# Kernel optimization log

Hardware: AMD Instinct MI355X
Metric: run time of the kernel (lower is better)

The kernel has to match this reference:

```python
import jax, jax.numpy as jnp
import numpy as np

N_HEAD = 16
NEG_BIG = 1e10  # matches the module's -10000000000.0 masking constant


def setup_inputs() -> dict:
    key = jax.random.key(0)
    k1, k2, k3 = jax.random.split(key, 3)
    B, S, D = 2, 2048, 1024
    std = 0.02
    return {
        "x": jax.random.normal(k1, (B, S, D), dtype=jnp.float32),
        "c_attn_w": jax.random.normal(k2, (D, 3 * D), dtype=jnp.float32) * std,
        "c_attn_b": jnp.zeros((3 * D,), dtype=jnp.float32),
        "c_proj_w": jax.random.normal(k3, (D, D), dtype=jnp.float32) * std,
        "c_proj_b": jnp.zeros((D,), dtype=jnp.float32),
    }


def reference(x, c_attn_w, c_attn_b, c_proj_w, c_proj_b):
    B, S, D = x.shape
    H = N_HEAD
    Dh = D // H

    # c_attn: fused QKV projection (Conv1D == linear)
    qkv = jnp.einsum("bsd,df->bsf", x, c_attn_w) + c_attn_b  # [B,S,3D]
    q, k, v = jnp.split(qkv, 3, axis=-1)

    def split_heads(t):  # [B,S,D] -> [B,H,S,Dh]
        return t.reshape(B, S, H, Dh).transpose(0, 2, 1, 3)

    q, k, v = split_heads(q), split_heads(k), split_heads(v)
    present = jnp.stack([k, v], axis=1)  # [B,2,H,S,Dh]

    # scores: explicit O(S^2) matrix, scaled by sqrt(head_dim)
    w = jnp.einsum("bhqd,bhkd->bhqk", q, k) / jnp.sqrt(
        jnp.asarray(Dh, dtype=q.dtype)
    )  # [B,H,S,S]

    # causal mask, applied exactly as in the source: w*mask - 1e10*(1-mask)
    mask = jnp.tril(jnp.ones((S, S), dtype=w.dtype))[None, None]  # [1,1,S,S]
    w = w * mask - NEG_BIG * (1.0 - mask)

    w = jax.nn.softmax(w, axis=-1)
    a = jnp.einsum("bhqk,bhkd->bhqd", w, v)  # [B,H,S,Dh]

    # merge heads: [B,H,S,Dh] -> [B,S,D]
    a = a.transpose(0, 2, 1, 3).reshape(B, S, D)

    # output projection
    a = jnp.einsum("bsd,df->bsf", a, c_proj_w) + c_proj_b
    return (a, present)
```

## Files before the change

kernel.cpp:

```cpp
#include <hip/hip_runtime.h>
#include <hip/hip_bf16.h>
#include <stdint.h>

typedef __bf16 bf16_t;
typedef __bf16 bf16x8 __attribute__((ext_vector_type(8)));
typedef __bf16 bf16x4v __attribute__((ext_vector_type(4)));
typedef float f32x4 __attribute__((ext_vector_type(4)));

#define MFMA16(A, B, C) __builtin_amdgcn_mfma_f32_16x16x32_bf16((A), (B), (C), 0, 0, 0)

#define BB 2
#define SS 2048
#define DD 1024
#define HH 16
#define DH 64
#define MM (BB * SS)

__device__ __forceinline__ void load_lds16(const void* g, void* l) {
  __builtin_amdgcn_global_load_lds(
      (const __attribute__((address_space(1))) void*)g,
      (__attribute__((address_space(3))) void*)l, 16, 0, 0);
}

__device__ __forceinline__ float fast_exp2(float x) {
  float r;
  asm("v_exp_f32 %0, %1" : "=v"(r) : "v"(x));
  return r;
}
__device__ __forceinline__ uint32_t cvt_pk_bf16(float lo, float hi) {
  uint32_t u;
  asm("v_cvt_pk_bf16_f32 %0, %1, %2" : "=v"(u) : "v"(lo), "v"(hi));
  return u;
}


__global__ __launch_bounds__(256) void cvt_f32_to_bf16(const float* __restrict__ in,
                                                       bf16_t* __restrict__ out, int n4) {
  int i = blockIdx.x * blockDim.x + threadIdx.x;
  if (i >= n4) return;
  float4 v = reinterpret_cast<const float4*>(in)[i];
  bf16x4v o;
  o[0] = (bf16_t)v.x; o[1] = (bf16_t)v.y; o[2] = (bf16_t)v.z; o[3] = (bf16_t)v.w;
  reinterpret_cast<bf16x4v*>(out)[i] = o;
}

__global__ void transpose_f32_to_bf16(const float* __restrict__ W, bf16_t* __restrict__ WT,
                                      int K, int N) {
  __shared__ float tile[32][33];
  int n0 = blockIdx.x * 32, k0 = blockIdx.y * 32;
  int tx = threadIdx.x, ty = threadIdx.y;
  #pragma unroll
  for (int i = ty; i < 32; i += 8) tile[i][tx] = W[(size_t)(k0 + i) * N + n0 + tx];
  __syncthreads();
  #pragma unroll
  for (int i = ty; i < 32; i += 8) WT[(size_t)(n0 + i) * K + k0 + tx] = (bf16_t)tile[tx][i];
}

template <int EPI>
__global__ __launch_bounds__(256) void gemm_bf16(
    const bf16_t* __restrict__ A, const bf16_t* __restrict__ BT,
    const float* __restrict__ bias, float* __restrict__ outf,
    bf16_t* __restrict__ q_b, bf16_t* __restrict__ k_b, bf16_t* __restrict__ vt_b,
    int M, int N, int K) {
  __shared__ __align__(16) bf16_t At[2][128 * 32];
  __shared__ __align__(16) bf16_t Bt[2][128 * 32];

  const int tid = threadIdx.x;
  const int l = tid & 63, w = tid >> 6;
  const int lr = l & 15, lg = l >> 4;
  const int wr = w >> 1, wc = w & 1;
  const int row0 = blockIdx.y * 128, col0 = blockIdx.x * 128;

  auto stage = [&](int buf, int k0) {
    #pragma unroll
    for (int i = 0; i < 2; ++i) {
      int e = (tid + i * 256) * 8;
      int r = e >> 5, c = e & 31;
      int base = (w * 64 + i * 256) * 8;
      load_lds16(&A[(size_t)(row0 + r) * K + k0 + c], &At[buf][base]);
      load_lds16(&BT[(size_t)(col0 + r) * K + k0 + c], &Bt[buf][base]);
    }
  };

  f32x4 vz = {0.f, 0.f, 0.f, 0.f};
  f32x4 acc[4][4];
  #pragma unroll
  for (int m = 0; m < 4; ++m)
    #pragma unroll
    for (int n = 0; n < 4; ++n) acc[m][n] = vz;

  stage(0, 0);
  __syncthreads();
  int cur = 0;
  for (int k0 = 0; k0 < K; k0 += 32) {
    if (k0 + 32 < K) stage(cur ^ 1, k0 + 32);
    bf16x8 af[4], bfr[4];
    #pragma unroll
    for (int m = 0; m < 4; ++m)
      af[m] = *(const bf16x8*)&At[cur][(wr * 64 + m * 16 + lr) * 32 + lg * 8];
    #pragma unroll
    for (int n = 0; n < 4; ++n)
      bfr[n] = *(const bf16x8*)&Bt[cur][(wc * 64 + n * 16 + lr) * 32 + lg * 8];
    #pragma unroll
    for (int m = 0; m < 4; ++m)
      #pragma unroll
      for (int n = 0; n < 4; ++n) acc[m][n] = MFMA16(af[m], bfr[n], acc[m][n]);
    __syncthreads();
    cur ^= 1;
  }

  #pragma unroll
  for (int m = 0; m < 4; ++m) {
    int rl = wr * 64 + m * 16 + lg * 4;
    #pragma unroll
    for (int n = 0; n < 4; ++n) {
      int col = col0 + wc * 64 + n * 16 + lr;
      float bz = bias[col];
      #pragma unroll
      for (int r = 0; r < 4; ++r) {
        int row = row0 + rl + r;
        float v = acc[m][n][r] + bz;
        if (EPI == 1) {
          outf[(size_t)row * N + col] = v;
        } else {
          int b = row >> 11, s = row & 2047;
          int part = col >> 10, d = col & 1023;
          int h = d >> 6, dh = d & 63;
          size_t idx = ((size_t)(b * HH + h) * SS + s) * DH + dh;
          if (part == 0) {
            q_b[idx] = (bf16_t)v;
          } else if (part == 1) {
            k_b[idx] = (bf16_t)v;
            outf[(((size_t)(b * 2 + 0) * HH + h) * SS + s) * DH + dh] = v;
          } else {
            vt_b[((size_t)(b * HH + h) * DH + dh) * SS + s] = (bf16_t)v;
            outf[(((size_t)(b * 2 + 1) * HH + h) * SS + s) * DH + dh] = v;
          }
        }
      }
    }
  }
}

__global__ __launch_bounds__(256) void attn_fwd(
    const bf16_t* __restrict__ q_b, const bf16_t* __restrict__ k_b,
    const bf16_t* __restrict__ vt_b, bf16_t* __restrict__ attn_out) {
  __shared__ __align__(16) bf16_t Kt[2][64 * 64];
  __shared__ __align__(16) bf16_t Vt[2][64 * 64];
  __shared__ __align__(16) bf16_t P_lds[4][32][72];

  const int bh = blockIdx.y;
  const int q0b = (gridDim.x - 1 - blockIdx.x) * 128;
  const int tid = threadIdx.x;
  const int w = tid >> 6, l = tid & 63;
  const int lr = l & 15, lg = l >> 4;

  const bf16_t* qb = q_b + (size_t)bh * SS * DH;
  const bf16_t* kb = k_b + (size_t)bh * SS * DH;
  const bf16_t* vt = vt_b + (size_t)bh * DH * SS;

  const int r0 = tid >> 3;
  const int cs = (((tid & 7) * 16) ^ ((r0 & 7) << 4)) >> 1;
  const bf16_t* gk0 = kb + r0 * DH + cs;
  const bf16_t* gk1 = gk0 + 32 * DH;
  const bf16_t* gv0 = vt + (size_t)r0 * SS + cs;
  const bf16_t* gv1 = gv0 + 32 * SS;
  auto stageKV = [&](int buf) {
    bf16_t* lk = &Kt[buf][w * 512];
    load_lds16(gk0, lk);
    load_lds16(gk1, lk + 2048);
    bf16_t* lv = &Vt[buf][w * 512];
    load_lds16(gv0, lv);
    load_lds16(gv1, lv + 2048);
    gk0 += 64 * DH; gk1 += 64 * DH; gv0 += 64; gv1 += 64;
  };

  const int qrow0 = q0b + w * 32 + lr;
  const int qrow1 = qrow0 + 16;
  bf16x8 qf[2][2];
  qf[0][0] = *(const bf16x8*)&qb[(size_t)qrow0 * DH + lg * 8];
  qf[0][1] = *(const bf16x8*)&qb[(size_t)qrow0 * DH + 32 + lg * 8];
  qf[1][0] = *(const bf16x8*)&qb[(size_t)qrow1 * DH + lg * 8];
  qf[1][1] = *(const bf16x8*)&qb[(size_t)qrow1 * DH + 32 + lg * 8];

  bf16x8 ones;
  #pragma unroll
  for (int j = 0; j < 8; ++j) ones[j] = (bf16_t)1.0f;

  f32x4 vzero = {0.f, 0.f, 0.f, 0.f};
  f32x4 oacc[2][4];
  #pragma unroll
  for (int q = 0; q < 2; ++q)
    #pragma unroll
    for (int d = 0; d < 4; ++d) oacc[q][d] = vzero;
  float m_run[2] = {-1e30f, -1e30f}, l_run[2] = {0.f, 0.f};

  const float SCL = 0.125f * 1.4426950408889634f;
  const int sw = (lr & 7) << 4;
  const int rd0 = (lg * 16) ^ sw;
  const int rd1 = (64 + lg * 16) ^ sw;

  const int nkv = q0b / 64 + 2;
  stageKV(0);
  __syncthreads();
  int cur = 0;
  for (int t = 0; t < nkv; ++t) {
    const int kv0 = t * 64;
    if (t + 1 < nkv) stageKV(cur ^ 1);

    float sc[2][4][4];
    #pragma unroll
    for (int kvf = 0; kvf < 4; ++kvf) {
      const char* kbase = (const char*)&Kt[cur][0] + (kvf * 16 + lr) * 128;
      bf16x8 kf0 = *(const bf16x8*)(kbase + rd0);
      bf16x8 kf1 = *(const bf16x8*)(kbase + rd1);
      #pragma unroll
      for (int q = 0; q < 2; ++q) {
        f32x4 a = vzero;
        a = MFMA16(kf0, qf[q][0], a);
        a = MFMA16(kf1, qf[q][1], a);
        #pragma unroll
        for (int r = 0; r < 4; ++r) sc[q][kvf][r] = a[r];
      }
    }
    if (kv0 + 63 > q0b + w * 32) {
      #pragma unroll
      for (int q = 0; q < 2; ++q) {
        int dthr = (q ? qrow1 : qrow0) - kv0;
        #pragma unroll
        for (int kvf = 0; kvf < 4; ++kvf)
          #pragma unroll
          for (int r = 0; r < 4; ++r) {
            int kvl = kvf * 16 + lg * 4 + r;
            if (kvl > dthr) sc[q][kvf][r] = -1e30f;
          }
      }
    }

    #pragma unroll
    for (int q = 0; q < 2; ++q) {
      float tm = fmaxf(fmaxf(sc[q][0][0], sc[q][0][1]), sc[q][0][2]);
      tm = fmaxf(fmaxf(tm, sc[q][0][3]), sc[q][1][0]);
      tm = fmaxf(fmaxf(tm, sc[q][1][1]), sc[q][1][2]);
      tm = fmaxf(fmaxf(tm, sc[q][1][3]), sc[q][2][0]);
      tm = fmaxf(fmaxf(tm, sc[q][2][1]), sc[q][2][2]);
      tm = fmaxf(fmaxf(tm, sc[q][2][3]), sc[q][3][0]);
      tm = fmaxf(fmaxf(tm, sc[q][3][1]), sc[q][3][2]);
      tm = fmaxf(tm, sc[q][3][3]);
      tm = fmaxf(tm, __shfl_xor(tm, 16));
      tm = fmaxf(tm, __shfl_xor(tm, 32));
      if (!__all(tm <= m_run[q] + 44.0f)) {
        float mnew = fmaxf(m_run[q], tm);
        float alpha = fast_exp2((m_run[q] - mnew) * SCL);
        l_run[q] *= alpha;
        #pragma unroll
        for (int d = 0; d < 4; ++d) oacc[q][d] *= alpha;
        m_run[q] = mnew;
      }
      float mneg = m_run[q] * (-SCL);
      #pragma unroll
      for (int kvf = 0; kvf < 4; ++kvf) {
        float p0 = fast_exp2(__builtin_fmaf(sc[q][kvf][0], SCL, mneg));
        float p1 = fast_exp2(__builtin_fmaf(sc[q][kvf][1], SCL, mneg));
        float p2 = fast_exp2(__builtin_fmaf(sc[q][kvf][2], SCL, mneg));
        float p3 = fast_exp2(__builtin_fmaf(sc[q][kvf][3], SCL, mneg));
        uint2 pk;
        pk.x = cvt_pk_bf16(p0, p1);
        pk.y = cvt_pk_bf16(p2, p3);
        *(uint2*)&P_lds[w][q * 16 + lr][kvf * 16 + lg * 4] = pk;
      }
    }

    bf16x8 pf[2][2];
    #pragma unroll
    for (int q = 0; q < 2; ++q) {
      pf[q][0] = *(const bf16x8*)&P_lds[w][q * 16 + lr][lg * 8];
      pf[q][1] = *(const bf16x8*)&P_lds[w][q * 16 + lr][32 + lg * 8];
      f32x4 ls = vzero;
      ls = MFMA16(ones, pf[q][0], ls);
      ls = MFMA16(ones, pf[q][1], ls);
      l_run[q] += ls[0];
    }
    #pragma unroll
    for (int d = 0; d < 4; ++d) {
      const char* vbase = (const char*)&Vt[cur][0] + (d * 16 + lr) * 128;
      bf16x8 vf0 = *(const bf16x8*)(vbase + rd0);
      bf16x8 vf1 = *(const bf16x8*)(vbase + rd1);
      #pragma unroll
      for (int q = 0; q < 2; ++q) {
        oacc[q][d] = MFMA16(vf0, pf[q][0], oacc[q][d]);
        oacc[q][d] = MFMA16(vf1, pf[q][1], oacc[q][d]);
      }
    }
    __syncthreads();
    cur ^= 1;
  }

  const int b = bh >> 4, h = bh & 15;
  #pragma unroll
  for (int q = 0; q < 2; ++q) {
    float inv_l = 1.f / l_run[q];
    int qrow = q ? qrow1 : qrow0;
    #pragma unroll
    for (int d = 0; d < 4; ++d)
      #pragma unroll
      for (int r = 0; r < 4; ++r) {
        int dd = d * 16 + lg * 4 + r;
        attn_out[((size_t)(b * SS + qrow)) * DD + h * DH + dd] =
            (bf16_t)(oacc[q][d][r] * inv_l);
      }
  }
}

extern "C" void kernel_launch(void* const* d_in, const int* in_sizes, int n_in,
                              void* d_out, int out_size, void* d_ws, size_t ws_size,
                              hipStream_t stream) {
  const float* x = (const float*)d_in[0];
  const float* c_attn_w = (const float*)d_in[1];
  const float* c_attn_b = (const float*)d_in[2];
  const float* c_proj_w = (const float*)d_in[3];
  const float* c_proj_b = (const float*)d_in[4];

  float* out = (float*)d_out;
  float* present = out + (size_t)BB * SS * DD;

  char* ws = (char*)d_ws;
  bf16_t* xb     = (bf16_t*)(ws + 0);
  bf16_t* wqkvT  = (bf16_t*)(ws + 8388608);
  bf16_t* wprojT = (bf16_t*)(ws + 14680064);
  bf16_t* q_b    = (bf16_t*)(ws + 16777216);
  bf16_t* k_b    = (bf16_t*)(ws + 25165824);
  bf16_t* vt_b   = (bf16_t*)(ws + 33554432);
  bf16_t* attn_o = (bf16_t*)(ws + 41943040);

  cvt_f32_to_bf16<<<(MM * DD / 4 + 255) / 256, 256, 0, stream>>>(x, xb, MM * DD / 4);
  transpose_f32_to_bf16<<<dim3(3 * DD / 32, DD / 32), dim3(32, 8), 0, stream>>>(
      c_attn_w, wqkvT, DD, 3 * DD);
  transpose_f32_to_bf16<<<dim3(DD / 32, DD / 32), dim3(32, 8), 0, stream>>>(
      c_proj_w, wprojT, DD, DD);
  gemm_bf16<0><<<dim3(3 * DD / 128, MM / 128), 256, 0, stream>>>(
      xb, wqkvT, c_attn_b, present, q_b, k_b, vt_b, MM, 3 * DD, DD);
  attn_fwd<<<dim3(SS / 128, BB * HH), 256, 0, stream>>>(q_b, k_b, vt_b, attn_o);
  gemm_bf16<1><<<dim3(DD / 128, MM / 128), 256, 0, stream>>>(
      attn_o, wprojT, c_proj_b, out, nullptr, nullptr, nullptr, MM, DD, DD);
}
```

Before: 228.2 us.

## Rewrite GEMMs with larger templated tiles, BK=64, XOR-swizzled LDS, and 512 threads

Replaces the fixed 128x128x32 GEMM with a templated kernel that uses 512-thread blocks, a BK of 64, and an XOR swizzle on LDS rows to avoid bank conflicts. The QKV projection now uses 256x192 tiles and the output projection uses 128x128 tiles with 8 waves. Larger tiles give more reuse per load and fewer K-loop synchronisations, at the cost of more LDS and registers per block and fewer blocks overall. The attention kernel also raises wave priority around its PV MFMA section.

New measurement: 225.2 us. Within noise of the previous version (-1.3%).

```diff
diff --git a/kernel.cpp b/kernel.cpp
--- a/kernel.cpp
+++ b/kernel.cpp
@@ -56,65 +56,89 @@
   for (int i = ty; i < 32; i += 8) WT[(size_t)(n0 + i) * K + k0 + tx] = (bf16_t)tile[tx][i];
 }
 
-template <int EPI>
-__global__ __launch_bounds__(256) void gemm_bf16(
+template <int BM, int BN, int WGM, int WGN, int EPI>
+__global__ __launch_bounds__(512) void gemm2(
     const bf16_t* __restrict__ A, const bf16_t* __restrict__ BT,
     const float* __restrict__ bias, float* __restrict__ outf,
     bf16_t* __restrict__ q_b, bf16_t* __restrict__ k_b, bf16_t* __restrict__ vt_b,
     int M, int N, int K) {
-  __shared__ __align__(16) bf16_t At[2][128 * 32];
-  __shared__ __align__(16) bf16_t Bt[2][128 * 32];
+  constexpr int BK = 64;
+  constexpr int MF = BM / WGM / 16;
+  constexpr int NF = BN / WGN / 16;
+  constexpr int RS = BM / WGM;
+  constexpr int CS = BN / WGN;
+  constexpr int LA = BM * BK * 2 / (512 * 16);
+  constexpr int LB = BN * BK * 2 / (512 * 16);
+
+  __shared__ __align__(16) bf16_t At[2][BM * BK];
+  __shared__ __align__(16) bf16_t Bt[2][BN * BK];
 
   const int tid = threadIdx.x;
   const int l = tid & 63, w = tid >> 6;
   const int lr = l & 15, lg = l >> 4;
-  const int wr = w >> 1, wc = w & 1;
-  const int row0 = blockIdx.y * 128, col0 = blockIdx.x * 128;
+  const int wr = w / WGN, wc = w % WGN;
+  const int row0 = blockIdx.y * BM, col0 = blockIdx.x * BN;
 
   auto stage = [&](int buf, int k0) {
     #pragma unroll
-    for (int i = 0; i < 2; ++i) {
-      int e = (tid + i * 256) * 8;
-      int r = e >> 5, c = e & 31;
-      int base = (w * 64 + i * 256) * 8;
-      load_lds16(&A[(size_t)(row0 + r) * K + k0 + c], &At[buf][base]);
-      load_lds16(&BT[(size_t)(col0 + r) * K + k0 + c], &Bt[buf][base]);
+    for (int i = 0; i < LA; ++i) {
+      int e = (tid + i * 512) * 8;
+      int r = e >> 6, c = e & 63;
+      int cs = ((c * 2) ^ ((r & 7) << 4)) >> 1;
+      load_lds16(&A[(size_t)(row0 + r) * K + k0 + cs], &At[buf][(w * 64 + i * 512) * 8]);
+    }
+    #pragma unroll
+    for (int i = 0; i < LB; ++i) {
+      int e = (tid + i * 512) * 8;
+      int r = e >> 6, c = e & 63;
+      int cs = ((c * 2) ^ ((r & 7) << 4)) >> 1;
+      load_lds16(&BT[(size_t)(col0 + r) * K + k0 + cs], &Bt[buf][(w * 64 + i * 512) * 8]);
     }
   };
 
   f32x4 vz = {0.f, 0.f, 0.f, 0.f};
-  f32x4 acc[4][4];
-  #pragma unroll
-  for (int m = 0; m < 4; ++m)
-    #pragma unroll
-    for (int n = 0; n < 4; ++n) acc[m][n] = vz;
-
+  f32x4 acc[MF][NF];
+  #pragma unroll
+  for (int m = 0; m < MF; ++m)
+    #pragma unroll
+    for (int n = 0; n < NF; ++n) acc[m][n] = vz;
+
+  const int sw = (lr & 7) << 4;
+  const int nk = K / BK;
   stage(0, 0);
   __syncthreads();
   int cur = 0;
-  for (int k0 = 0; k0 < K; k0 += 32) {
-    if (k0 + 32 < K) stage(cur ^ 1, k0 + 32);
-    bf16x8 af[4], bfr[4];
-    #pragma unroll
-    for (int m = 0; m < 4; ++m)
-      af[m] = *(const bf16x8*)&At[cur][(wr * 64 + m * 16 + lr) * 32 + lg * 8];
-    #pragma unroll
-    for (int n = 0; n < 4; ++n)
-      bfr[n] = *(const bf16x8*)&Bt[cur][(wc * 64 + n * 16 + lr) * 32 + lg * 8];
-    #pragma unroll
-    for (int m = 0; m < 4; ++m)
-      #pragma unroll
-      for (int n = 0; n < 4; ++n) acc[m][n] = MFMA16(af[m], bfr[n], acc[m][n]);
+  for (int k = 0; k < nk; ++k) {
+    if (k + 1 < nk) stage(cur ^ 1, (k + 1) * BK);
+    #pragma unroll
+    for (int kk = 0; kk < 2; ++kk) {
+      const int rdo = (kk * 64 + lg * 16) ^ sw;
+      bf16x8 af[MF], bfr[NF];
+      #pragma unroll
+      for (int m = 0; m < MF; ++m) {
+        int row = wr * RS + m * 16 + lr;
+        af[m] = *(const bf16x8*)((const char*)&At[cur][0] + row * 128 + rdo);
+      }
+      #pragma unroll
+      for (int n = 0; n < NF; ++n) {
+        int brow = wc * CS + n * 16 + lr;
+        bfr[n] = *(const bf16x8*)((const char*)&Bt[cur][0] + brow * 128 + rdo);
+      }
+      #pragma unroll
+      for (int m = 0; m < MF; ++m)
+        #pragma unroll
+        for (int n = 0; n < NF; ++n) acc[m][n] = MFMA16(af[m], bfr[n], acc[m][n]);
+    }
     __syncthreads();
     cur ^= 1;
   }
 
   #pragma unroll
-  for (int m = 0; m < 4; ++m) {
-    int rl = wr * 64 + m * 16 + lg * 4;
-    #pragma unroll
-    for (int n = 0; n < 4; ++n) {
-      int col = col0 + wc * 64 + n * 16 + lr;
+  for (int m = 0; m < MF; ++m) {
+    int rl = wr * RS + m * 16 + lg * 4;
+    #pragma unroll
+    for (int n = 0; n < NF; ++n) {
+      int col = col0 + wc * CS + n * 16 + lr;
       float bz = bias[col];
       #pragma unroll
       for (int r = 0; r < 4; ++r) {
@@ -281,6 +305,7 @@
       ls = MFMA16(ones, pf[q][1], ls);
       l_run[q] += ls[0];
     }
+    __builtin_amdgcn_s_setprio(1);
     #pragma unroll
     for (int d = 0; d < 4; ++d) {
       const char* vbase = (const char*)&Vt[cur][0] + (d * 16 + lr) * 128;
@@ -292,6 +317,7 @@
         oacc[q][d] = MFMA16(vf1, pf[q][1], oacc[q][d]);
       }
     }
+    __builtin_amdgcn_s_setprio(0);
     __syncthreads();
     cur ^= 1;
   }
@@ -338,9 +364,9 @@
       c_attn_w, wqkvT, DD, 3 * DD);
   transpose_f32_to_bf16<<<dim3(DD / 32, DD / 32), dim3(32, 8), 0, stream>>>(
       c_proj_w, wprojT, DD, DD);
-  gemm_bf16<0><<<dim3(3 * DD / 128, MM / 128), 256, 0, stream>>>(
+  gemm2<256, 192, 4, 2, 0><<<dim3(3 * DD / 192, MM / 256), 512, 0, stream>>>(
       xb, wqkvT, c_attn_b, present, q_b, k_b, vt_b, MM, 3 * DD, DD);
   attn_fwd<<<dim3(SS / 128, BB * HH), 256, 0, stream>>>(q_b, k_b, vt_b, attn_o);
-  gemm_bf16<1><<<dim3(DD / 128, MM / 128), 256, 0, stream>>>(
+  gemm2<128, 128, 2, 4, 1><<<dim3(DD / 128, MM / 128), 512, 0, stream>>>(
       attn_o, wprojT, c_proj_b, out, nullptr, nullptr, nullptr, MM, DD, DD);
 }
```
